# Kernel tuning notes

Hardware: AMD Instinct MI355X
Metric: run time of the kernel (lower is better)

## Reference

```python
import jax, jax.numpy as jnp
import numpy as np

HEADS = 8


def _ln(x, g, b):
    m = x.mean(-1, keepdims=True)
    v = ((x - m) ** 2).mean(-1, keepdims=True)
    return (x - m) / jnp.sqrt(v + 1e-5) * g + b


def _mha(xq, xkv, inw, inb, outw, outb):
    # torch nn.MultiheadAttention (dropout off). xq/xkv: [B,S,D]
    B, S, D = xq.shape
    hd = D // HEADS
    q = (xq @ inw[:D].T + inb[:D]).reshape(B, S, HEADS, hd)
    k = (xkv @ inw[D:2 * D].T + inb[D:2 * D]).reshape(B, S, HEADS, hd)
    v = (xkv @ inw[2 * D:].T + inb[2 * D:]).reshape(B, S, HEADS, hd)
    s = jnp.einsum('bqhd,bkhd->bhqk', q, k) / np.float32(np.sqrt(hd))
    o = jnp.einsum('bhqk,bkhd->bqhd', jax.nn.softmax(s, axis=-1), v).reshape(B, S, D)
    return o @ outw.T + outb


def _eca(x1, x2, qw, qb, kw, kb, vw, vb):
    # EfficientCrossAttention: bmm -> clamp -> softmax -> bmm
    Q = x1 @ qw.T + qb
    K = x2 @ kw.T + kb
    V = x2 @ vw.T + vb
    s = jnp.einsum('bqd,bkd->bqk', Q, K) / np.float32(np.sqrt(Q.shape[-1]))
    s = jnp.clip(s, -100.0, 100.0)
    return jnp.einsum('bqk,bkd->bqd', jax.nn.softmax(s, axis=-1), V)


def _itda(img, caps, qw, qb, kw, kb, vw, vb):
    B, NC, D = caps.shape
    S = img.shape[1]  # 196
    cap_e = jnp.broadcast_to(caps[:, :, None, :], (B, NC, S, D)).reshape(B * NC, S, D)
    img_e = jnp.broadcast_to(img[:, None, :, :], (B, NC, S, D)).reshape(B * NC, S, D)
    out = _eca(cap_e, img_e, qw, qb, kw, kb, vw, vb).reshape(B, NC, S, D)
    mask = (caps.sum(-1) != 0).astype(out.dtype)[:, :, None, None]  # [B,NC,1,1]
    msum = jnp.clip(jnp.broadcast_to(mask, (B, NC, S, 1)).sum(1), 1e-6, None)
    return (out * mask).sum(1) / msum


def _mse(a, b):
    return jnp.mean((a - b) ** 2)


def _forward(input_1, input_2, cap1, cap2, img_w, img_b, w_emb, h_emb,
             mlp_w1, mlp_b1, mlp_w2, mlp_b2, fc_w, fc_b, efc_w, efc_b,
             efc2_w, efc2_b, tr_in_w, tr_in_b, tr_out_w, tr_out_b,
             tr_ln_g, tr_ln_b, itda_qw, itda_qb, itda_kw, itda_kb, itda_vw, itda_vb,
             ca_qw, ca_qb, ca_kw, ca_kb, ca_vw, ca_vb,
             sa_qw, sa_qb, sa_kw, sa_kb, sa_vw, sa_vb):
    B, C, H, W = input_1.shape
    A = img_w.shape[0]
    # caption projections
    cap1_o = cap1 @ fc_w.T + fc_b  # [B,NC,512]
    cap2_o = cap2 @ fc_w.T + fc_b
    cap1_m = jnp.broadcast_to(cap1_o.mean(1)[:, None, :], (B, H * W, A))
    cap2_m = jnp.broadcast_to(cap2_o.mean(1)[:, None, :], (B, H * W, A))
    # 1x1 conv + positional embedding; pe[i,j] = [w_emb[j], h_emb[i]]
    pe = jnp.concatenate([jnp.broadcast_to(w_emb[None, :, :], (W, W, A // 2)),
                          jnp.broadcast_to(h_emb[:, None, :], (H, H, A // 2))], axis=-1)

    def embed(x):
        y = jnp.einsum('bchw,ac->bhwa', x, img_w) + img_b + pe
        return y.reshape(B, H * W, A)

    x1 = embed(input_1)  # [B,196,512]
    x2 = embed(input_2)
    # CDCR (Barlow-Twins style) loss

    def mlp(x):
        return jax.nn.relu(x @ mlp_w1.T + mlp_b1) @ mlp_w2.T + mlp_b2

    f1 = mlp(x1.reshape(-1, A))
    f2 = mlp(x2.reshape(-1, A))
    z_a = (f1 - f1.mean(0)) / jnp.std(f1, axis=0, ddof=1)
    z_b = (f2 - f2.mean(0)) / jnp.std(f2, axis=0, ddof=1)
    Bt, D = z_a.shape
    c = (z_a.T @ z_b) / Bt
    on_diag = jnp.sum((jnp.diagonal(c) - 1.0) ** 2)
    off_diag = jnp.sum(c.reshape(-1)[1:].reshape(D - 1, D + 1)[:, :-1] ** 2)
    cdcr_loss = on_diag + 0.003 * off_diag
    # cross-transformer stack (simultaneous update, as in torch tuple RHS)
    h1, h2 = x1, x2
    for l in range(tr_in_w.shape[0]):
        def layer(q, kv):
            a = _mha(q, kv, tr_in_w[l], tr_in_b[l], tr_out_w[l], tr_out_b[l])
            return _ln(q + a, tr_ln_g[l], tr_ln_b[l])
        h1, h2 = layer(h1, h2), layer(h2, h1)
    diff1 = x1 - h1
    diff2 = x2 - h2
    # ITDA module
    c12 = _eca(diff1, diff2, ca_qw, ca_qb, ca_kw, ca_kb, ca_vw, ca_vb)
    c21 = _eca(diff2, diff1, ca_qw, ca_qb, ca_kw, ca_kb, ca_vw, ca_vb)
    s11 = _eca(diff1, diff1, sa_qw, sa_qb, sa_kw, sa_kb, sa_vw, sa_vb)
    s22 = _eca(diff2, diff2, sa_qw, sa_qb, sa_kw, sa_kb, sa_vw, sa_vb)
    d_bef = _itda(diff1, cap2_o, itda_qw, itda_qb, itda_kw, itda_kb, itda_vw, itda_vb)
    d_aft = _itda(diff2, cap1_o, itda_qw, itda_qb, itda_kw, itda_kb, itda_vw, itda_vb)
    s_bef = _itda(diff1, cap1_o, itda_qw, itda_qb, itda_kw, itda_kb, itda_vw, itda_vb)
    s_aft = _itda(diff2, cap2_o, itda_qw, itda_qb, itda_kw, itda_kb, itda_vw, itda_vb)
    img_to_txt_loss = _mse(d_bef, c12) + _mse(d_aft, c21) + _mse(s_bef, s11) + _mse(s_aft, s22)

    def efc(x):
        return jax.nn.relu(x @ efc_w.T + efc_b)

    dyn = efc(jnp.concatenate([d_bef, d_aft], -1))
    sta = efc(jnp.concatenate([s_bef, s_aft], -1))
    align = efc(jnp.concatenate([dyn, sta], -1))
    txt = efc(jnp.concatenate([cap1_m, cap2_m], -1))
    comb = jnp.concatenate([diff1, diff2, txt, align], -1)  # [B,196,2048]
    out = jax.nn.relu(comb @ efc2_w.T + efc2_b)
    return out, cdcr_loss, img_to_txt_loss


def setup_inputs() -> dict:
    key = jax.random.key(0)
    ks = iter(jax.random.split(key, 64))

    def nrm(shape, s=0.02):
        return jax.random.normal(next(ks), shape, jnp.float32) * s

    B, C, H, W, NC, A = 64, 1024, 14, 14, 16, 512
    inp = dict(
        input_1=jax.random.normal(next(ks), (B, C, H, W), jnp.float32),
        input_2=jax.random.normal(next(ks), (B, C, H, W), jnp.float32),
        cap1=jax.random.normal(next(ks), (B, NC, 768), jnp.float32),
        cap2=jax.random.normal(next(ks), (B, NC, 768), jnp.float32),
        img_w=nrm((A, C)), img_b=jnp.zeros((A,), jnp.float32),
        w_emb=nrm((14, A // 2)), h_emb=nrm((14, A // 2)),
        mlp_w1=nrm((4 * A, A)), mlp_b1=jnp.zeros((4 * A,), jnp.float32),
        mlp_w2=nrm((A, 4 * A)), mlp_b2=jnp.zeros((A,), jnp.float32),
        fc_w=nrm((A, 768)), fc_b=jnp.zeros((A,), jnp.float32),
        efc_w=nrm((A, 2 * A)), efc_b=jnp.zeros((A,), jnp.float32),
        efc2_w=nrm((A, 4 * A)), efc2_b=jnp.zeros((A,), jnp.float32),
        tr_in_w=nrm((2, 3 * A, A)), tr_in_b=jnp.zeros((2, 3 * A), jnp.float32),
        tr_out_w=nrm((2, A, A)), tr_out_b=jnp.zeros((2, A), jnp.float32),
        tr_ln_g=jnp.ones((2, A), jnp.float32), tr_ln_b=jnp.zeros((2, A), jnp.float32),
    )
    for pfx in ('itda', 'ca', 'sa'):
        for nm in ('q', 'k', 'v'):
            inp[pfx + '_' + nm + 'w'] = nrm((A, A))
            inp[pfx + '_' + nm + 'b'] = jnp.zeros((A,), jnp.float32)
    return inp


def reference(input_1, input_2, cap1, cap2, img_w, img_b, w_emb, h_emb,
              mlp_w1, mlp_b1, mlp_w2, mlp_b2, fc_w, fc_b, efc_w, efc_b,
              efc2_w, efc2_b, tr_in_w, tr_in_b, tr_out_w, tr_out_b,
              tr_ln_g, tr_ln_b, itda_qw, itda_qb, itda_kw, itda_kb, itda_vw, itda_vb,
              ca_qw, ca_qb, ca_kw, ca_kb, ca_vw, ca_vb,
              sa_qw, sa_qb, sa_kw, sa_kb, sa_vw, sa_vb):
    return _forward(input_1, input_2, cap1, cap2, img_w, img_b, w_emb, h_emb,
                    mlp_w1, mlp_b1, mlp_w2, mlp_b2, fc_w, fc_b, efc_w, efc_b,
                    efc2_w, efc2_b, tr_in_w, tr_in_b, tr_out_w, tr_out_b,
                    tr_ln_g, tr_ln_b, itda_qw, itda_qb, itda_kw, itda_kb, itda_vw, itda_vb,
                    ca_qw, ca_qb, ca_kw, ca_kb, ca_vw, ca_vb,
                    sa_qw, sa_qb, sa_kw, sa_kb, sa_vw, sa_vb)
```

## Files before the change

kernel.cpp:

```cpp
#include <hip/hip_runtime.h>
#include <hip/hip_bf16.h>
#include <stdint.h>
#include <math.h>

#define BB   64
#define SS   196
#define BS   12544
#define NOUT 6422528L
#define SLD  224

typedef __attribute__((ext_vector_type(8))) short bf16x8;
typedef __attribute__((ext_vector_type(4))) float f32x4;

__device__ __forceinline__ float block_red256(float v, float* red, bool ismax) {
#pragma unroll
  for (int o = 32; o > 0; o >>= 1) {
    float t = __shfl_down(v, o, 64);
    v = ismax ? fmaxf(v, t) : v + t;
  }
  int lane = threadIdx.x & 63, wid = threadIdx.x >> 6;
  if (lane == 0) red[wid] = v;
  __syncthreads();
  float r = ismax ? fmaxf(fmaxf(red[0], red[1]), fmaxf(red[2], red[3]))
                  : (red[0] + red[1]) + (red[2] + red[3]);
// ... 47 lines not shown
  f32x4 acc[4][4] = {};
  float4 xa[4], xw[4], ya[4], yw[4];

  auto ldt = [&](float4 (&ta)[4], float4 (&tw)[4], int t) {
    const float* ap = Ap + t * 32;
    const float* wp = Wp + t * 32;
#pragma unroll
    for (int i = 0; i < 4; ++i) {
      ta[i] = *(const float4*)(ap + i * 4);
      tw[i] = *(const float4*)(wp + i * 4);
    }
  };
  auto stage = [&](float4 (&ta)[4], float4 (&tw)[4], int p) {
    cvt8(&As[p][srow][skh], ta[0], ta[1]);
    cvt8(&As[p][srow][skh + 8], ta[2], ta[3]);
    cvt8(&Bs[p][srow][skh], tw[0], tw[1]);
    cvt8(&Bs[p][srow][skh + 8], tw[2], tw[3]);
  };
  auto step = [&](int t, float4 (&la)[4], float4 (&lw)[4],
                  float4 (&ca)[4], float4 (&cw)[4]) {
    const int par = t & 1;
    if (t + 2 < NK) ldt(la, lw, t + 2);
    bf16x8 af[4], bfr[4];
#pragma unroll
    for (int i = 0; i < 4; ++i) af[i] = *(const bf16x8*)&As[par][wm * 64 + i * 16 + fr][fq * 8];
#pragma unroll
    for (int j = 0; j < 4; ++j) bfr[j] = *(const bf16x8*)&Bs[par][wn * 64 + j * 16 + fr][fq * 8];
    if (t + 1 < NK) stage(ca, cw, par ^ 1);
#pragma unroll
    for (int i = 0; i < 4; ++i)
#pragma unroll
      for (int j = 0; j < 4; ++j)
        acc[i][j] = __builtin_amdgcn_mfma_f32_16x16x32_bf16(af[i], bfr[j], acc[i][j], 0, 0, 0);
    lds_barrier();
  };

  ldt(xa, xw, 0);
  stage(xa, xw, 0);
  if (NK > 1) ldt(xa, xw, 1);
  lds_barrier();
  int t = 0;
  for (; t + 1 < NK; t += 2) { step(t, ya, yw, xa, xw); step(t + 1, xa, xw, ya, yw); }
  if (t < NK) step(t, ya, yw, xa, xw);

  short* Cs = (short*)C;
#pragma unroll
  for (int i = 0; i < 4; ++i) {
    int mB = m0 + wm * 64 + i * 16 + fq * 4;
#pragma unroll
    for (int j = 0; j < 4; ++j) {
      int n = n0 + wn * 64 + j * 16 + fr;
      float bz = bias[n];
#pragma unroll
      for (int r2 = 0; r2 < 4; ++r2) {
        float v = acc[i][j][r2] + bz;
        if (relu) v = fmaxf(v, 0.f);
        if (obf) Cs[(long)(mB + r2) * N + n] = f2bf(v);
        else     C[(long)(mB + r2) * N + n] = v;
      }
    }
  }
}

__global__ __launch_bounds__(256) void k_mfma_embed(
    const float* __restrict__ X1, const float* __restrict__ X2,
    const float* __restrict__ W,
    const float* __restrict__ bias,
    const float* __restrict__ wemb, const float* __restrict__ hemb,
    float* __restrict__ C1, float* __restrict__ C2) {
  __shared__ short As[2][128][40];
  __shared__ short Bs[2][128][40];
  const float* X = blockIdx.z ? X2 : X1;
  float* C = blockIdx.z ? C2 : C1;
  const int tid = threadIdx.x;
  const int lane = tid & 63, wave = tid >> 6;
  const int wm = wave >> 1, wn = wave & 1;
  const int NX = gridDim.x;
  const int wg = xcd_swizzle(blockIdx.y * NX + blockIdx.x, NX * gridDim.y);
  const int m0 = (wg / NX) * 128, n0 = (wg % NX) * 128;
  const int K = 1024, N = 512;
  const int srow = tid >> 1, skh = (tid & 1) * 16;
  const float* Wp = W + (long)(n0 + srow) * K + skh;
  const int arow = tid & 127, khalf = tid >> 7;
  const int am = m0 + arow;
  const int ab = am / 196, as_ = am % 196;
  const float* Xp = X + (long)ab * 200704 + as_;
  const int fr = lane & 15, fq = lane >> 4;
  const int NK = K >> 5;
  f32x4 acc[4][4] = {};
  float xx[16], yx[16];
  float4 xw[4], yw[4];

  auto ldt = [&](float (&tx)[16], float4 (&tw)[4], int t) {
    const int kb = t * 32 + khalf * 16;
#pragma unroll
    for (int i = 0; i < 16; ++i) tx[i] = Xp[(long)(kb + i) * 196];
    const float* wp = Wp + t * 32;
#pragma unroll
    for (int i = 0; i < 4; ++i) tw[i] = *(const float4*)(wp + i * 4);
  };
  auto stage = [&](float (&tx)[16], float4 (&tw)[4], int p) {
    union { short s[16]; int4 v[2]; } u;
#pragma unroll
    for (int i = 0; i < 16; ++i) u.s[i] = f2bf(tx[i]);
    int4* dst = (int4*)&As[p][arow][khalf * 16];
    dst[0] = u.v[0]; dst[1] = u.v[1];
    cvt8(&Bs[p][srow][skh], tw[0], tw[1]);
    cvt8(&Bs[p][srow][skh + 8], tw[2], tw[3]);
  };
  auto step = [&](int t, float (&lx)[16], float4 (&lw)[4],
                  float (&cx)[16], float4 (&cw)[4]) {
    const int par = t & 1;
    if (t + 2 < NK) ldt(lx, lw, t + 2);
    bf16x8 af[4], bfr[4];
#pragma unroll
    for (int i = 0; i < 4; ++i) af[i] = *(const bf16x8*)&As[par][wm * 64 + i * 16 + fr][fq * 8];
#pragma unroll
    for (int j = 0; j < 4; ++j) bfr[j] = *(const bf16x8*)&Bs[par][wn * 64 + j * 16 + fr][fq * 8];
    if (t + 1 < NK) stage(cx, cw, par ^ 1);
#pragma unroll
    for (int i = 0; i < 4; ++i)
#pragma unroll
      for (int j = 0; j < 4; ++j)
        acc[i][j] = __builtin_amdgcn_mfma_f32_16x16x32_bf16(af[i], bfr[j], acc[i][j], 0, 0, 0);
    lds_barrier();
  };

  ldt(xx, xw, 0);
  stage(xx, xw, 0);
  if (NK > 1) ldt(xx, xw, 1);
  lds_barrier();
  int t = 0;
  for (; t + 1 < NK; t += 2) { step(t, yx, yw, xx, xw); step(t + 1, xx, xw, yx, yw); }
  if (t < NK) step(t, yx, yw, xx, xw);

#pragma unroll
  for (int i = 0; i < 4; ++i) {
    int mB = m0 + wm * 64 + i * 16 + fq * 4;
#pragma unroll
    for (int j = 0; j < 4; ++j) {
      int n = n0 + wn * 64 + j * 16 + fr;
      float bz = bias[n];
#pragma unroll
      for (int r2 = 0; r2 < 4; ++r2) {
        int m = mB + r2;
        int s = m % 196;
        float pe = (n < 256) ? wemb[(s % 14) * 256 + n] : hemb[(s / 14) * 256 + (n - 256)];
        C[(long)m * N + n] = acc[i][j][r2] + bz + pe;
      }
    }
  }
}

__global__ __launch_bounds__(256) void k_fmha_bf(
    const short* __restrict__ Q, const short* __restrict__ KV,
    float* __restrict__ O) {
  __shared__ short Vt[64][240];
  __shared__ short Pt[4][16][40];
  const int tid = threadIdx.x;
  const int lane = tid & 63, wave = tid >> 6;
  const int b = blockIdx.x, h = blockIdx.y;
  const long brow = (long)b * 196;
  const short* Qb = Q + brow * 512 + h * 64;
  const short* Kb = KV + brow * 1024 + h * 64;
  const short* Vb = KV + brow * 1024 + 512 + h * 64;
  float* Ob = O + brow * 512 + h * 64;
  const int fr = lane & 15, fq = lane >> 4;

  for (int i = tid; i < 64 * 32; i += 256) {
    int d = i >> 5, k = 192 + (i & 31);
    if (k >= 196) Vt[d][k] = 0;
  }
  for (int i = tid; i < 196 * 8; i += 256) {
    int s = i >> 3, c8 = (i & 7) * 8;
    bf16x8 v = *(const bf16x8*)(Vb + (long)s * 1024 + c8);
#pragma unroll
    for (int j = 0; j < 8; ++j) Vt[c8 + j][s] = v[j];
  }
  __syncthreads();

  for (int qt = wave; qt < 13; qt += 4) {
    const int q0 = qt * 16;
    const int qr = (q0 + fr < 196) ? q0 + fr : 195;
    const short* qp = Qb + (long)qr * 512 + fq * 8;
    bf16x8 aq0 = *(const bf16x8*)(qp);
    bf16x8 aq1 = *(const bf16x8*)(qp + 32);
    f32x4 sc[13];
#pragma unroll
    for (int t = 0; t < 13; ++t) {
      int kr = (t * 16 + fr < 196) ? t * 16 + fr : 195;
      const short* kp = Kb + (long)kr * 1024 + fq * 8;
      bf16x8 bk0 = *(const bf16x8*)(kp);
      bf16x8 bk1 = *(const bf16x8*)(kp + 32);
      f32x4 z = {};
      z = __builtin_amdgcn_mfma_f32_16x16x32_bf16(aq0, bk0, z, 0, 0, 0);
      z = __builtin_amdgcn_mfma_f32_16x16x32_bf16(aq1, bk1, z, 0, 0, 0);
      sc[t] = z;
    }
#pragma unroll
    for (int t = 0; t < 13; ++t)
#pragma unroll
      for (int r2 = 0; r2 < 4; ++r2) sc[t][r2] *= 0.125f;
    if (fr >= 4) {
#pragma unroll
      for (int r2 = 0; r2 < 4; ++r2) sc[12][r2] = -1e30f;
    }
#pragma unroll
    for (int r2 = 0; r2 < 4; ++r2) {
      float m = sc[0][r2];
#pragma unroll
      for (int t = 1; t < 13; ++t) m = fmaxf(m, sc[t][r2]);
#pragma unroll
      for (int o = 1; o < 16; o <<= 1) m = fmaxf(m, __shfl_xor(m, o, 64));
      float s = 0.f;
#pragma unroll
      for (int t = 0; t < 13; ++t) { float e = expf(sc[t][r2] - m); sc[t][r2] = e; s += e; }
#pragma unroll
      for (int o = 1; o < 16; o <<= 1) s += __shfl_xor(s, o, 64);
      float inv = 1.0f / s;
#pragma unroll
      for (int t = 0; t < 13; ++t) sc[t][r2] *= inv;
    }
    f32x4 acc_o[4] = {};
#pragma unroll
    for (int s7 = 0; s7 < 7; ++s7) {
      const int t0 = 2 * s7, t1 = 2 * s7 + 1;
#pragma unroll
      for (int r2 = 0; r2 < 4; ++r2) {
        Pt[wave][fq * 4 + r2][fr] = f2bf(sc[t0][r2]);
        Pt[wave][fq * 4 + r2][16 + fr] = (t1 < 13) ? f2bf(sc[t1][r2]) : (short)0;
      }
      asm volatile("s_waitcnt lgkmcnt(0)" ::: "memory");
      bf16x8 ap = *(const bf16x8*)&Pt[wave][fr][fq * 8];
#pragma unroll
      for (int dt = 0; dt < 4; ++dt) {
        bf16x8 bv = *(const bf16x8*)&Vt[dt * 16 + fr][32 * s7 + fq * 8];
        acc_o[dt] = __builtin_amdgcn_mfma_f32_16x16x32_bf16(ap, bv, acc_o[dt], 0, 0, 0);
      }
    }
#pragma unroll
    for (int r2 = 0; r2 < 4; ++r2) {
      int qrow = q0 + fq * 4 + r2;
      if (qrow < 196) {
        float* op = Ob + (long)qrow * 512;
#pragma unroll
        for (int dt = 0; dt < 4; ++dt) op[dt * 16 + fr] = acc_o[dt][r2];
      }
    }
  }
}

__global__ __launch_bounds__(256) void k_mfma_bnt(
    const float* __restrict__ A, const float* __restrict__ B, float* __restrict__ C,
    int M, int N, int K, int lda, int ldb, int ldc, int nz2,
    int64_t sA1, int64_t sA2, int64_t sB1, int64_t sB2, int64_t sC1, int64_t sC2,
    float scale, int clampf, const float* __restrict__ bias2, int relu2) {
  __shared__ short As[2][64][40];
  __shared__ short Bs[2][64][40];
  const int tid = threadIdx.x;
  const int lane = tid & 63, wave = tid >> 6;
  const int NX = gridDim.x;
  const int wg = xcd_swizzle(blockIdx.y * NX + blockIdx.x, NX * gridDim.y);
  const int m0 = (wg / NX) * 64, n0 = (wg % NX) * 64;
  const int z = blockIdx.z, z1 = z / nz2, z2 = z % nz2;
  const float* Ab = A + z1 * sA1 + z2 * sA2;
  const float* Bb = B + z1 * sB1 + z2 * sB2;
  float* Cb = C + z1 * sC1 + z2 * sC2;
  const int sr = tid >> 2, skh = (tid & 3) * 8;
  const int ar = (m0 + sr < M) ? m0 + sr : M - 1;
  const int br = (n0 + sr < N) ? n0 + sr : N - 1;
  const float* Ap = Ab + (long)ar * lda + skh;
  const float* Bp = Bb + (long)br * ldb + skh;
  const int fr = lane & 15, fq = lane >> 4;
  const int NK = K >> 5;
  f32x4 acc[4] = {};
  float4 xa[2], xb[2], ya[2], yb[2];

  auto ldt = [&](float4 (&ta)[2], float4 (&tb)[2], int t) {
    const int kb = t * 32;
#pragma unroll
    for (int i = 0; i < 2; ++i) {
      ta[i] = *(const float4*)(Ap + kb + i * 4);
      tb[i] = *(const float4*)(Bp + kb + i * 4);
    }
  };
  auto stage = [&](float4 (&ta)[2], float4 (&tb)[2], int p) {
    cvt8(&As[p][sr][skh], ta[0], ta[1]);
    cvt8(&Bs[p][sr][skh], tb[0], tb[1]);
  };
  auto step = [&](int t, float4 (&la)[2], float4 (&lb)[2],
                  float4 (&ca)[2], float4 (&cb)[2]) {
    const int par = t & 1;
    if (t + 2 < NK) ldt(la, lb, t + 2);
    bf16x8 bfr = *(const bf16x8*)&Bs[par][wave * 16 + fr][fq * 8];
    bf16x8 af[4];
#pragma unroll
    for (int i = 0; i < 4; ++i) af[i] = *(const bf16x8*)&As[par][i * 16 + fr][fq * 8];
    if (t + 1 < NK) stage(ca, cb, par ^ 1);
#pragma unroll
    for (int i = 0; i < 4; ++i)
      acc[i] = __builtin_amdgcn_mfma_f32_16x16x32_bf16(af[i], bfr, acc[i], 0, 0, 0);
    lds_barrier();
  };

  ldt(xa, xb, 0);
  stage(xa, xb, 0);
  if (NK > 1) ldt(xa, xb, 1);
  lds_barrier();
  int t = 0;
  for (; t + 1 < NK; t += 2) { step(t, ya, yb, xa, xb); step(t + 1, xa, xb, ya, yb); }
  if (t < NK) step(t, ya, yb, xa, xb);

  const int n = n0 + wave * 16 + fr;
  if (n < N) {
    float bz = bias2 ? bias2[n] : 0.f;
#pragma unroll
    for (int i = 0; i < 4; ++i) {
      int mb = m0 + i * 16 + fq * 4;
#pragma unroll
      for (int r2 = 0; r2 < 4; ++r2) {
        int m = mb + r2;
        if (m < M) {
          float v = acc[i][r2] * scale + bz;
          if (relu2) v = fmaxf(v, 0.f);
          if (clampf) v = fminf(fmaxf(v, -100.f), 100.f);
          Cb[(long)m * ldc + n] = v;
        }
      }
    }
  }
}

__global__ __launch_bounds__(256) void k_mfma_bnt_abf(
    const short* __restrict__ A, const float* __restrict__ B, float* __restrict__ C,
    int M, int N, int K, int lda, int ldb, int ldc,
    const float* __restrict__ bias2, int relu2) {
  __shared__ short As[2][64][40];
  __shared__ short Bs[2][64][40];
  const int tid = threadIdx.x;
  const int lane = tid & 63, wave = tid >> 6;
  const int NX = gridDim.x;
  const int wg = xcd_swizzle(blockIdx.y * NX + blockIdx.x, NX * gridDim.y);
  const int m0 = (wg / NX) * 64, n0 = (wg % NX) * 64;
  const int sr = tid >> 2, skh = (tid & 3) * 8;
  const int ar = (m0 + sr < M) ? m0 + sr : M - 1;
  const int br = (n0 + sr < N) ? n0 + sr : N - 1;
  const short* Ap = A + (long)ar * lda + skh;
  const float* Bp = B + (long)br * ldb + skh;
  const int fr = lane & 15, fq = lane >> 4;
  const int NK = K >> 5;
  f32x4 acc[4] = {};
  int4 xa, ya;
  float4 xb[2], yb[2];

  auto ldt = [&](int4& ta, float4 (&tb)[2], int t) {
    const int kb = t * 32;
    ta = *(const int4*)(Ap + kb);
#pragma unroll
    for (int i = 0; i < 2; ++i) tb[i] = *(const float4*)(Bp + kb + i * 4);
  };
  auto stage = [&](int4& ta, float4 (&tb)[2], int p) {
    *(int4*)&As[p][sr][skh] = ta;
    cvt8(&Bs[p][sr][skh], tb[0], tb[1]);
  };
  auto step = [&](int t, int4& la, float4 (&lb)[2], int4& ca, float4 (&cb)[2]) {
    const int par = t & 1;
    if (t + 2 < NK) ldt(la, lb, t + 2);
    bf16x8 bfr = *(const bf16x8*)&Bs[par][wave * 16 + fr][fq * 8];
    bf16x8 af[4];
#pragma unroll
    for (int i = 0; i < 4; ++i) af[i] = *(const bf16x8*)&As[par][i * 16 + fr][fq * 8];
    if (t + 1 < NK) stage(ca, cb, par ^ 1);
#pragma unroll
    for (int i = 0; i < 4; ++i)
      acc[i] = __builtin_amdgcn_mfma_f32_16x16x32_bf16(af[i], bfr, acc[i], 0, 0, 0);
    lds_barrier();
  };

  ldt(xa, xb, 0);
  stage(xa, xb, 0);
  if (NK > 1) ldt(xa, xb, 1);
  lds_barrier();
  int t = 0;
  for (; t + 1 < NK; t += 2) { step(t, ya, yb, xa, xb); step(t + 1, xa, xb, ya, yb); }
  if (t < NK) step(t, ya, yb, xa, xb);

  const int n = n0 + wave * 16 + fr;
  if (n < N) {
    float bz = bias2 ? bias2[n] : 0.f;
#pragma unroll
    for (int i = 0; i < 4; ++i) {
      int mb = m0 + i * 16 + fq * 4;
#pragma unroll
      for (int r2 = 0; r2 < 4; ++r2) {
        int m = mb + r2;
        if (m < M) {
          float v = acc[i][r2] + bz;
          if (relu2) v = fmaxf(v, 0.f);
          C[(long)m * ldc + n] = v;
// ... 188 lines not shown
}

__global__ void k_zero(float* __restrict__ p, int n) {
  int i = blockIdx.x * 256 + threadIdx.x;
  if (i < n) p[i] = 0.f;
}

__global__ __launch_bounds__(256) void k_diff(
    float* __restrict__ d, const float* __restrict__ x, const float* __restrict__ h) {
  long i = ((long)blockIdx.x * 256 + threadIdx.x) * 4;
  float4 xv = *(const float4*)(x + i);
  float4 hv = *(const float4*)(h + i);
  float4 r; r.x = xv.x - hv.x; r.y = xv.y - hv.y; r.z = xv.z - hv.z; r.w = xv.w - hv.w;
  *(float4*)(d + i) = r;
}

__global__ __launch_bounds__(256) void k_catkv(
    float* __restrict__ dw, const float* __restrict__ kw, const float* __restrict__ vw,
    float* __restrict__ db, const float* __restrict__ kb, const float* __restrict__ vb) {
  int i = blockIdx.x * 256 + threadIdx.x;
  int r = i >> 9;
  dw[i] = (r < 512) ? kw[i] : vw[i - 262144];
  if (i < 1024) db[i] = (i < 512) ? kb[i] : vb[i - 512];
}

__global__ __launch_bounds__(256) void k_colstats(
    const float* __restrict__ f, float* __restrict__ sums, float* __restrict__ sqs) {
  int c = blockIdx.x * 32 + (threadIdx.x & 31);
  int rbase = blockIdx.y * 256;
  int r0 = rbase + (threadIdx.x >> 5);
  float s = 0.f, s2 = 0.f;
  for (int r = r0; r < rbase + 256; r += 8) {
    float v = f[(long)r * 512 + c];
    s += v; s2 += v * v;
  }
  __shared__ float sh[256], sh2[256];
  sh[threadIdx.x] = s; sh2[threadIdx.x] = s2;
  __syncthreads();
  if (threadIdx.x < 32) {
    for (int i = 1; i < 8; ++i) { s += sh[i * 32 + threadIdx.x]; s2 += sh2[i * 32 + threadIdx.x]; }
    atomicAdd(&sums[c], s);
    atomicAdd(&sqs[c], s2);
  }
}

__global__ void k_finstats(const float* __restrict__ sums, const float* __restrict__ sqs,
                           float* __restrict__ mean, float* __restrict__ istd) {
  int c = blockIdx.x * 256 + threadIdx.x;
  float mu = sums[c] / 12544.0f;
  float var = (sqs[c] - 12544.0f * mu * mu) / 12543.0f;
  mean[c] = mu;
  istd[c] = 1.0f / sqrtf(var);
}

__global__ __launch_bounds__(256) void k_znorm(float* __restrict__ f, const float* __restrict__ mean,
                                               const float* __restrict__ istd) {
  long i = (long)blockIdx.x * 256 + threadIdx.x;
  int c = (int)(i & 511);
  f[i] = (f[i] - mean[c]) * istd[c];
}

__global__ __launch_bounds__(256) void k_cdcr_part(const float* __restrict__ Cm,
                                                   double* __restrict__ part) {
  int base = blockIdx.x * 1024;
  double on = 0, off = 0;
  for (int i = base + threadIdx.x; i < base + 1024; i += 256) {
    float v = Cm[i];
    int r = i >> 9, c = i & 511;
    if (r == c) { double d = (double)v - 1.0; on += d * d; }
    else        { off += (double)v * (double)v; }
  }
  __shared__ double s_on[256], s_off[256];
  s_on[threadIdx.x] = on; s_off[threadIdx.x] = off;
  __syncthreads();
  for (int st = 128; st > 0; st >>= 1) {
    if (threadIdx.x < st) { s_on[threadIdx.x] += s_on[threadIdx.x + st]; s_off[threadIdx.x] += s_off[threadIdx.x + st]; }
    __syncthreads();
  }
  if (threadIdx.x == 0) { part[blockIdx.x] = s_on[0]; part[256 + blockIdx.x] = s_off[0]; }
}

__global__ void k_cdcr_fin(const double* __restrict__ part, float* __restrict__ out) {
  __shared__ double s_on[256], s_off[256];
  s_on[threadIdx.x] = part[threadIdx.x];
  s_off[threadIdx.x] = part[256 + threadIdx.x];
  __syncthreads();
  for (int st = 128; st > 0; st >>= 1) {
    if (threadIdx.x < st) { s_on[threadIdx.x] += s_on[threadIdx.x + st]; s_off[threadIdx.x] += s_off[threadIdx.x + st]; }
    __syncthreads();
  }
  if (threadIdx.x == 0) out[0] = (float)(s_on[0] + 0.003 * s_off[0]);
}

__global__ __launch_bounds__(64) void k_mask(const float* __restrict__ capo, float* __restrict__ mask) {
  int pidx = blockIdx.x;
  float s = 0.f;
  for (int i = threadIdx.x; i < 512; i += 64) s += capo[(long)pidx * 512 + i];
#pragma unroll
  for (int o = 32; o > 0; o >>= 1) s += __shfl_down(s, o, 64);
  if (threadIdx.x == 0) mask[pidx] = (s != 0.f) ? 1.f : 0.f;
}

__global__ __launch_bounds__(256) void k_meannc(const float* __restrict__ src, const float* __restrict__ mask,
                                                float* __restrict__ vec) {
  int d = blockIdx.x * 256 + threadIdx.x;
  int b = blockIdx.y;
  float acc = 0.f, ms = 0.f;
  for (int nc = 0; nc < 16; ++nc) {
    float mk = mask ? mask[b * 16 + nc] : 1.f;
    acc += src[((long)b * 16 + nc) * 512 + d] * mk;
    ms += mk;
  }
  vec[(long)b * 512 + d] = acc / fmaxf(ms, 1e-6f);
}

__global__ __launch_bounds__(256) void k_mse(const float* __restrict__ full, const float* __restrict__ vec,
                                             double* __restrict__ part) {
  double loc = 0;
  const long n = NOUT;
  for (long i = (long)blockIdx.x * 256 + threadIdx.x; i < n; i += 256L * 1024) {
    int d = (int)(i & 511);
    int b = (int)(i >> 9) / 196;
    float df = full[i] - vec[b * 512 + d];
    loc += (double)df * (double)df;
  }
  __shared__ double sh[256];
  sh[threadIdx.x] = loc;
  __syncthreads();
  for (int st = 128; st > 0; st >>= 1) {
    if (threadIdx.x < st) sh[threadIdx.x] += sh[threadIdx.x + st];
    __syncthreads();
  }
  if (threadIdx.x == 0) part[blockIdx.x] = sh[0];
}

__global__ void k_finloss(const double* __restrict__ part, float* __restrict__ out) {
  __shared__ double sh[256];
  double s = 0;
  for (int i = threadIdx.x; i < 4096; i += 256) s += part[i];
  sh[threadIdx.x] = s;
  __syncthreads();
  for (int st = 128; st > 0; st >>= 1) {
    if (threadIdx.x < st) sh[threadIdx.x] += sh[threadIdx.x + st];
    __syncthreads();
  }
  if (threadIdx.x == 0) out[0] = (float)(sh[0] / (64.0 * 196.0 * 512.0));
}

__global__ __launch_bounds__(256) void k_concat2(float* __restrict__ dst, const float* __restrict__ a,
                                                 const float* __restrict__ b) {
  int i = blockIdx.x * 256 + threadIdx.x;
  int col = i & 1023, row = i >> 10;
  dst[i] = (col < 512) ? a[row * 512 + col] : b[row * 512 + col - 512];
}

__global__ __launch_bounds__(256) void k_comb_bf(
    short* __restrict__ dst, const float* __restrict__ d1, const float* __restrict__ d2,
    const float* __restrict__ txt, const float* __restrict__ al) {
  long i = (long)blockIdx.x * 256 + threadIdx.x;
  int col = (int)(i & 2047);
  long m = i >> 11;
  int b = (int)(m / 196);
  float v;
  if (col < 512)       v = d1[m * 512 + col];
  else if (col < 1024) v = d2[m * 512 + col - 512];
  else if (col < 1536) v = txt[(long)b * 512 + col - 1024];
  else                 v = al[(long)b * 512 + col - 1536];
  dst[i] = f2bf(v);
}

extern "C" void kernel_launch(void* const* d_in, const int* in_sizes, int n_in,
                              void* d_out, int out_size, void* d_ws, size_t ws_size,
                              hipStream_t stream) {
  (void)in_sizes; (void)n_in; (void)out_size; (void)ws_size;
  const float* in1    = (const float*)d_in[0];
  const float* in2    = (const float*)d_in[1];
  const float* cap1   = (const float*)d_in[2];
  const float* cap2   = (const float*)d_in[3];
  const float* imgw   = (const float*)d_in[4];
  const float* imgb   = (const float*)d_in[5];
  const float* wemb   = (const float*)d_in[6];
  const float* hemb   = (const float*)d_in[7];
  const float* mlpw1  = (const float*)d_in[8];
  const float* mlpb1  = (const float*)d_in[9];
  const float* mlpw2  = (const float*)d_in[10];
  const float* mlpb2  = (const float*)d_in[11];
  const float* fcw    = (const float*)d_in[12];
  const float* fcb    = (const float*)d_in[13];
  const float* efcw   = (const float*)d_in[14];
  const float* efcb   = (const float*)d_in[15];
  const float* efc2w  = (const float*)d_in[16];
  const float* efc2b  = (const float*)d_in[17];
  const float* trinw  = (const float*)d_in[18];
  const float* trinb  = (const float*)d_in[19];
  const float* troutw = (const float*)d_in[20];
  const float* troutb = (const float*)d_in[21];
  const float* trlng  = (const float*)d_in[22];
  const float* trlnb  = (const float*)d_in[23];
  const float* itqw = (const float*)d_in[24]; const float* itqb = (const float*)d_in[25];
  const float* itkw = (const float*)d_in[26]; const float* itkb = (const float*)d_in[27];
  const float* itvw = (const float*)d_in[28]; const float* itvb = (const float*)d_in[29];
  const float* caqw = (const float*)d_in[30]; const float* caqb = (const float*)d_in[31];
  const float* cakw = (const float*)d_in[32]; const float* cakb = (const float*)d_in[33];
  const float* cavw = (const float*)d_in[34]; const float* cavb = (const float*)d_in[35];
  const float* saqw = (const float*)d_in[36]; const float* saqb = (const float*)d_in[37];
  const float* sakw = (const float*)d_in[38]; const float* sakb = (const float*)d_in[39];
  const float* savw = (const float*)d_in[40]; const float* savb = (const float*)d_in[41];

  float* out = (float*)d_out;

  const size_t SZ = (size_t)BS * 512;
  float* w = (float*)d_ws;
  auto alloc = [&](size_t n) { float* p = w; w += n; return p; };
  float* h1 = alloc(SZ);
  float* h2 = alloc(SZ);
  float* tA = alloc(SZ);
  float* tB = alloc(SZ);
  float* tC = alloc(SZ);
  float* tD = alloc(SZ);
  float* sbuf = alloc(SZ);
  float* cap1o = alloc(64 * 16 * 512);
  float* cap2o = alloc(64 * 16 * 512);
  float* qc1   = alloc(64 * 16 * 512);
  float* qc2   = alloc(64 * 16 * 512);
  float* attb  = alloc(64 * 16 * 512);
  float* attb2 = alloc(64 * 16 * 512);
  float* cmat  = alloc(512 * 512);
  float* colsum1 = alloc(512); float* colsq1 = alloc(512);
  float* colsum2 = alloc(512); float* colsq2 = alloc(512);
  float* mean1 = alloc(512); float* istd1 = alloc(512);
  float* mean2 = alloc(512); float* istd2 = alloc(512);
  float* mask1 = alloc(1024); float* mask2 = alloc(1024);
  float* vdbef = alloc(64 * 512); float* vdaft = alloc(64 * 512);
  float* vsbef = alloc(64 * 512); float* vsaft = alloc(64 * 512);
  float* cm1 = alloc(64 * 512); float* cm2 = alloc(64 * 512);
  float* vdyn = alloc(64 * 512); float* vsta = alloc(64 * 512);
  float* valign = alloc(64 * 512); float* vtxt = alloc(64 * 512);
  float* ccat = alloc(64 * 1024);
  double* msepart = (double*)alloc(4096 * 2);
  double* cdcrpart = (double*)alloc(1024);
  float* itkvw = alloc(1024 * 512); float* itkvb = alloc(1024);
  float* cakvw = alloc(1024 * 512); float* cakvb = alloc(1024);
  float* sakvw = alloc(1024 * 512); float* sakvb = alloc(1024);
  float* x1 = alloc(2 * SZ);
  float* x2 = x1 + SZ;

  auto gemm = [&](const float* Aa, const float* Ww, const float* bb, float* Cc,
                  int M, int N, int K, int relu) {
    long g128 = ((M % 128) == 0 && (N % 128) == 0) ? (long)(N / 128) * (M / 128) : 0;
    if (g128 >= 784 && (K % 32) == 0)
      k_mfma_nt<<<dim3(N / 128, M / 128), 256, 0, stream>>>(Aa, Ww, bb, Cc, M, N, K, relu, 0);
    else
      k_mfma_bnt<<<dim3(N / 64, (M + 63) / 64, 1), 256, 0, stream>>>(
          Aa, Ww, Cc, M, N, K, K, K, N, 1,
          0, 0, 0, 0, 0, 0, 1.0f, 0, bb, relu);
  };
  const int64_t RB = (int64_t)SS * 512;
  const int64_t QB = 16 * 512;
  auto attn512 = [&](const float* Qp, int64_t qZ1, int64_t qZ2, const float* KVp, int64_t kvZ,
                     float* Op, int64_t oZ1, int64_t oZ2, int M, int zq, float scale) {
    int mt = (M + 63) / 64;
    int64_t sS2 = (int64_t)M * SLD;
    int64_t sS1 = 64 * sS2;
    k_mfma_bnt<<<dim3(4, mt, 64 * zq), 256, 0, stream>>>(
        Qp, KVp, sbuf, M, 196, 512, 512, 1024, SLD, 64,
        qZ1, qZ2, 0, kvZ, sS1, sS2, scale, 1, nullptr, 0);
    k_softmax_rows<<<(64 * zq * M + 3) / 4, 256, 0, stream>>>(sbuf, 64 * zq * M);
    k_mfma_bnn<<<dim3(8, mt, 64 * zq), 256, 0, stream>>>(
        sbuf, KVp + 512, Op, M, 512, SLD, 196, SLD, 1024, 512, 64,
        sS1, sS2, 0, kvZ, oZ1, oZ2);
  };
  auto attn_mha = [&](const short* Qp, const short* KVp, float* Op) {
    k_fmha_bf<<<dim3(64, 8), 256, 0, stream>>>(Qp, KVp, Op);
  };
  auto efc64 = [&](const float* Aa, float* Cc) {
    k_mfma_bnt<<<dim3(8, 1, 1), 256, 0, stream>>>(
        Aa, efcw, Cc, 64, 512, 1024, 1024, 1024, 512, 1,
        0, 0, 0, 0, 0, 0, 1.0f, 0, efcb, 1);
  };

  const float scalE = 1.0f / sqrtf(512.0f);

  k_catkv<<<2048, 256, 0, stream>>>(itkvw, itkw, itvw, itkvb, itkb, itvb);
  k_catkv<<<2048, 256, 0, stream>>>(cakvw, cakw, cavw, cakvb, cakb, cavb);
  k_catkv<<<2048, 256, 0, stream>>>(sakvw, sakw, savw, sakvb, sakb, savb);

  k_mfma_embed<<<dim3(4, BS / 128, 2), 256, 0, stream>>>(
      in1, in2, imgw, imgb, wemb, hemb, x1, x2);
  gemm(cap1, fcw, fcb, cap1o, 1024, 512, 768, 0);
  gemm(cap2, fcw, fcb, cap2o, 1024, 512, 768, 0);
  k_meannc<<<dim3(2, 64), 256, 0, stream>>>(cap1o, nullptr, cm1);
  k_meannc<<<dim3(2, 64), 256, 0, stream>>>(cap2o, nullptr, cm2);

  k_mfma_nt<<<dim3(16, 98), 256, 0, stream>>>(x1, mlpw1, mlpb1, tC, BS, 2048, 512, 1, 1);
  k_mfma_bnt_abf<<<dim3(8, 196), 256, 0, stream>>>(
      (const short*)tC, mlpw2, tA, BS, 512, 2048, 2048, 2048, 512, mlpb2, 0);
  k_mfma_nt<<<dim3(16, 98), 256, 0, stream>>>(x2, mlpw1, mlpb1, tC, BS, 2048, 512, 1, 1);
  k_mfma_bnt_abf<<<dim3(8, 196), 256, 0, stream>>>(
      (const short*)tC, mlpw2, tB, BS, 512, 2048, 2048, 2048, 512, mlpb2, 0);
  k_zero<<<8, 256, 0, stream>>>(colsum1, 2048);
  k_colstats<<<dim3(16, 49), 256, 0, stream>>>(tA, colsum1, colsq1);
  k_colstats<<<dim3(16, 49), 256, 0, stream>>>(tB, colsum2, colsq2);
  k_finstats<<<2, 256, 0, stream>>>(colsum1, colsq1, mean1, istd1);
  k_finstats<<<2, 256, 0, stream>>>(colsum2, colsq2, mean2, istd2);
  k_znorm<<<25088, 256, 0, stream>>>(tA, mean1, istd1);
  k_znorm<<<25088, 256, 0, stream>>>(tB, mean2, istd2);
  k_zero<<<1024, 256, 0, stream>>>(cmat, 262144);
  k_mfma_corr<<<dim3(8, 8, 14), 256, 0, stream>>>(tA, tB, cmat, BS / 14, 1.0f / (float)BS);
  k_cdcr_part<<<256, 256, 0, stream>>>(cmat, cdcrpart);
  k_cdcr_fin<<<1, 256, 0, stream>>>(cdcrpart, out + NOUT);

  for (int l = 0; l < 2; ++l) {
    const float* Wq = trinw + (size_t)l * 1536 * 512;
    const float* Wkv = Wq + 512 * 512;
    const float* bq = trinb + l * 1536;
    const float* bkv = bq + 512;
    const float* Wo = troutw + (size_t)l * 512 * 512;
    const float* bo = troutb + l * 512;
    const float* g  = trlng + l * 512;
    const float* be = trlnb + l * 512;
    const float* s1 = l ? h1 : x1;
    const float* s2 = l ? h2 : x2;
    k_mfma_nt<<<dim3(4, 196), 256, 0, stream>>>(s1, Wq, bq, tA, 2 * BS, 512, 512, 0, 1);
    k_mfma_nt<<<dim3(8, 98), 256, 0, stream>>>(s2, Wkv, bkv, tC, BS, 1024, 512, 0, 1);
    k_mfma_nt<<<dim3(8, 98), 256, 0, stream>>>(s1, Wkv, bkv, tD, BS, 1024, 512, 0, 1);
    attn_mha((const short*)tA, (const short*)tC, tB);
    k_mfma_bnt<<<dim3(8, 196, 1), 256, 0, stream>>>(tB, Wo, sbuf, BS, 512, 512, 512, 512, 512, 1,
                                                    0, 0, 0, 0, 0, 0, 1.0f, 0, bo, 0);
    k_addln2<<<BS, 256, 0, stream>>>(h1, s1, sbuf, g, be);
    attn_mha((const short*)tA + (size_t)BS * 512, (const short*)tD, tB);
    k_mfma_bnt<<<dim3(8, 196, 1), 256, 0, stream>>>(tB, Wo, sbuf, BS, 512, 512, 512, 512, 512, 1,
                                                    0, 0, 0, 0, 0, 0, 1.0f, 0, bo, 0);
    k_addln2<<<BS, 256, 0, stream>>>(h2, s2, sbuf, g, be);
  }

  k_diff<<<12544, 256, 0, stream>>>(tC, x1, h1);

  gemm(cap1o, itqw, itqb, qc1, 2048, 512, 512, 0);
  k_mask<<<1024, 64, 0, stream>>>(cap1o, mask1);
  k_mask<<<1024, 64, 0, stream>>>(cap2o, mask2);
  gemm(tC, itkvw, itkvb, tA, BS, 1024, 512, 0);
  attn512(qc1, 524288, QB, tA, 2 * RB, attb, 524288, QB, 16, 2, scalE);
  k_meannc<<<dim3(2, 64), 256, 0, stream>>>(attb,  mask1, vsbef);
  k_meannc<<<dim3(2, 64), 256, 0, stream>>>(attb2, mask2, vdbef);
  gemm(tD, itkvw, itkvb, tA, BS, 1024, 512, 0);
  attn512(qc1, 524288, QB, tA, 2 * RB, attb, 524288, QB, 16, 2, scalE);
  k_meannc<<<dim3(2, 64), 256, 0, stream>>>(attb,  mask1, vdaft);
  k_meannc<<<dim3(2, 64), 256, 0, stream>>>(attb2, mask2, vsaft);

  auto eca_mse = [&](const float* xq, const float* xkv,
                     const float* qw2, const float* qb2,
                     const float* kvw2, const float* kvb2,
                     const float* vec, double* part) {
    gemm(xq,  qw2, qb2, h1, BS, 512, 512, 0);
    gemm(xkv, kvw2, kvb2, tA, BS, 1024, 512, 0);
    attn512(h1, 0, RB, tA, 2 * RB, h2, 0, RB, 196, 1, scalE);
    k_mse<<<1024, 256, 0, stream>>>(h2, vec, part);
  };
  eca_mse(tC, tD, caqw, caqb, cakvw, cakvb, vdbef, msepart);
  eca_mse(tD, tC, caqw, caqb, cakvw, cakvb, vdaft, msepart + 1024);
  eca_mse(tC, tC, saqw, saqb, sakvw, sakvb, vsbef, msepart + 2048);
  eca_mse(tD, tD, saqw, saqb, sakvw, sakvb, vsaft, msepart + 3072);
  k_finloss<<<1, 256, 0, stream>>>(msepart, out + NOUT + 1);

  k_concat2<<<256, 256, 0, stream>>>(ccat, vdbef, vdaft);
  efc64(ccat, vdyn);
  k_concat2<<<256, 256, 0, stream>>>(ccat, vsbef, vsaft);
  efc64(ccat, vsta);
  k_concat2<<<256, 256, 0, stream>>>(ccat, vdyn, vsta);
  efc64(ccat, valign);
  k_concat2<<<256, 256, 0, stream>>>(ccat, cm1, cm2);
  efc64(ccat, vtxt);

  k_comb_bf<<<100352, 256, 0, stream>>>((short*)h1, tC, tD, vtxt, valign);
  k_mfma_bnt_abf<<<dim3(8, 196), 256, 0, stream>>>(
      (const short*)h1, efc2w, out, BS, 512, 2048, 2048, 2048, 512, efc2b, 1);
}
```

Measured before the change: 2.383 ms.

## Batch paired branches into double-size GEMMs and attention launches

Merges the two image branches into single launches: the MLP, the KV projection, MHA (a z-dimension selects the KV source), the output projection, the add+LN, the ITDA KV GEMM, and the ECA pairs. The three independent efc GEMMs are stacked into one M=192 launch. MHA now writes bf16 output, which the bf16-A GEMM consumes, halving that intermediate's traffic. This cuts launch count and raises per-launch parallelism, at the cost of heavy buffer aliasing (negative strides, reused workspace regions) that is easy to get wrong.

```diff
diff --git a/kernel.cpp b/kernel.cpp
--- a/kernel.cpp
+++ b/kernel.cpp
@@ -223,19 +223,21 @@
   }
 }
 
-__global__ __launch_bounds__(256) void k_fmha_bf(
-    const short* __restrict__ Q, const short* __restrict__ KV,
-    float* __restrict__ O) {
+__global__ __launch_bounds__(256) void k_fmha_bf2(
+    const short* __restrict__ Q, const short* __restrict__ KVd1,
+    const short* __restrict__ KVd2, short* __restrict__ O) {
   __shared__ short Vt[64][240];
   __shared__ short Pt[4][16][40];
   const int tid = threadIdx.x;
   const int lane = tid & 63, wave = tid >> 6;
-  const int b = blockIdx.x, h = blockIdx.y;
+  const int b = blockIdx.x, h = blockIdx.y, z = blockIdx.z;
+  const short* KV = z ? KVd2 : KVd1;
   const long brow = (long)b * 196;
-  const short* Qb = Q + brow * 512 + h * 64;
+  const size_t zo = (size_t)z * BS * 512;
+  const short* Qb = Q + zo + brow * 512 + h * 64;
   const short* Kb = KV + brow * 1024 + h * 64;
   const short* Vb = KV + brow * 1024 + 512 + h * 64;
-  float* Ob = O + brow * 512 + h * 64;
+  short* Ob = O + zo + brow * 512 + h * 64;
   const int fr = lane & 15, fq = lane >> 4;
 
   for (int i = tid; i < 64 * 32; i += 256) {
@@ -263,10 +265,10 @@
       const short* kp = Kb + (long)kr * 1024 + fq * 8;
       bf16x8 bk0 = *(const bf16x8*)(kp);
       bf16x8 bk1 = *(const bf16x8*)(kp + 32);
-      f32x4 z = {};
-      z = __builtin_amdgcn_mfma_f32_16x16x32_bf16(aq0, bk0, z, 0, 0, 0);
-      z = __builtin_amdgcn_mfma_f32_16x16x32_bf16(aq1, bk1, z, 0, 0, 0);
-      sc[t] = z;
+      f32x4 zz = {};
+      zz = __builtin_amdgcn_mfma_f32_16x16x32_bf16(aq0, bk0, zz, 0, 0, 0);
+      zz = __builtin_amdgcn_mfma_f32_16x16x32_bf16(aq1, bk1, zz, 0, 0, 0);
+      sc[t] = zz;
     }
 #pragma unroll
     for (int t = 0; t < 13; ++t)
@@ -313,9 +315,9 @@
     for (int r2 = 0; r2 < 4; ++r2) {
       int qrow = q0 + fq * 4 + r2;
       if (qrow < 196) {
-        float* op = Ob + (long)qrow * 512;
-#pragma unroll
-        for (int dt = 0; dt < 4; ++dt) op[dt * 16 + fr] = acc_o[dt][r2];
+        short* op = Ob + (long)qrow * 512;
+#pragma unroll
+        for (int dt = 0; dt < 4; ++dt) op[dt * 16 + fr] = f2bf(acc_o[dt][r2]);
       }
     }
   }
@@ -810,6 +812,19 @@
   int i = blockIdx.x * 256 + threadIdx.x;
   int col = i & 1023, row = i >> 10;
   dst[i] = (col < 512) ? a[row * 512 + col] : b[row * 512 + col - 512];
+}
+
+__global__ __launch_bounds__(256) void k_concat6(
+    float* __restrict__ dst,
+    const float* __restrict__ a0, const float* __restrict__ b0,
+    const float* __restrict__ a1, const float* __restrict__ b1,
+    const float* __restrict__ a2, const float* __restrict__ b2) {
+  int i = blockIdx.x * 256 + threadIdx.x;
+  int col = i & 1023, row = i >> 10;
+  int grp = row >> 6, r = row & 63;
+  const float* a = grp == 0 ? a0 : (grp == 1 ? a1 : a2);
+  const float* b = grp == 0 ? b0 : (grp == 1 ? b1 : b2);
+  dst[i] = (col < 512) ? a[r * 512 + col] : b[r * 512 + col - 512];
 }
 
 __global__ __launch_bounds__(256) void k_comb_bf(
@@ -868,6 +883,7 @@
   float* out = (float*)d_out;
 
   const size_t SZ = (size_t)BS * 512;
+  const int64_t SZl = (int64_t)SZ;
   float* w = (float*)d_ws;
   auto alloc = [&](size_t n) { float* p = w; w += n; return p; };
   float* h1 = alloc(SZ);
@@ -893,8 +909,8 @@
   float* vsbef = alloc(64 * 512); float* vsaft = alloc(64 * 512);
   float* cm1 = alloc(64 * 512); float* cm2 = alloc(64 * 512);
   float* vdyn = alloc(64 * 512); float* vsta = alloc(64 * 512);
-  float* valign = alloc(64 * 512); float* vtxt = alloc(64 * 512);
-  float* ccat = alloc(64 * 1024);
+  float* vtxt = alloc(64 * 512); float* valign = alloc(64 * 512);
+  float* ccat = alloc(192 * 1024);
   double* msepart = (double*)alloc(4096 * 2);
   double* cdcrpart = (double*)alloc(1024);
   float* itkvw = alloc(1024 * 512); float* itkvb = alloc(1024);
@@ -915,25 +931,23 @@
   };
   const int64_t RB = (int64_t)SS * 512;
   const int64_t QB = 16 * 512;
-  auto attn512 = [&](const float* Qp, int64_t qZ1, int64_t qZ2, const float* KVp, int64_t kvZ,
+  auto attn512 = [&](const float* Qp, int64_t qZ1, int64_t qZ2,
+                     const float* KVp, int64_t kvZ1, int64_t kvZ2,
                      float* Op, int64_t oZ1, int64_t oZ2, int M, int zq, float scale) {
     int mt = (M + 63) / 64;
     int64_t sS2 = (int64_t)M * SLD;
     int64_t sS1 = 64 * sS2;
     k_mfma_bnt<<<dim3(4, mt, 64 * zq), 256, 0, stream>>>(
         Qp, KVp, sbuf, M, 196, 512, 512, 1024, SLD, 64,
-        qZ1, qZ2, 0, kvZ, sS1, sS2, scale, 1, nullptr, 0);
+        qZ1, qZ2, kvZ1, kvZ2, sS1, sS2, scale, 1, nullptr, 0);
     k_softmax_rows<<<(64 * zq * M + 3) / 4, 256, 0, stream>>>(sbuf, 64 * zq * M);
     k_mfma_bnn<<<dim3(8, mt, 64 * zq), 256, 0, stream>>>(
         sbuf, KVp + 512, Op, M, 512, SLD, 196, SLD, 1024, 512, 64,
-        sS1, sS2, 0, kvZ, oZ1, oZ2);
-  };
-  auto attn_mha = [&](const short* Qp, const short* KVp, float* Op) {
-    k_fmha_bf<<<dim3(64, 8), 256, 0, stream>>>(Qp, KVp, Op);
-  };
-  auto efc64 = [&](const float* Aa, float* Cc) {
-    k_mfma_bnt<<<dim3(8, 1, 1), 256, 0, stream>>>(
-        Aa, efcw, Cc, 64, 512, 1024, 1024, 1024, 512, 1,
+        sS1, sS2, kvZ1, kvZ2, oZ1, oZ2);
+  };
+  auto efcM = [&](const float* Aa, float* Cc, int M) {
+    k_mfma_bnt<<<dim3(8, (M + 63) / 64, 1), 256, 0, stream>>>(
+        Aa, efcw, Cc, M, 512, 1024, 1024, 1024, 512, 1,
         0, 0, 0, 0, 0, 0, 1.0f, 0, efcb, 1);
   };
 
@@ -950,21 +964,18 @@
   k_meannc<<<dim3(2, 64), 256, 0, stream>>>(cap1o, nullptr, cm1);
   k_meannc<<<dim3(2, 64), 256, 0, stream>>>(cap2o, nullptr, cm2);
 
-  k_mfma_nt<<<dim3(16, 98), 256, 0, stream>>>(x1, mlpw1, mlpb1, tC, BS, 2048, 512, 1, 1);
-  k_mfma_bnt_abf<<<dim3(8, 196), 256, 0, stream>>>(
-      (const short*)tC, mlpw2, tA, BS, 512, 2048, 2048, 2048, 512, mlpb2, 0);
-  k_mfma_nt<<<dim3(16, 98), 256, 0, stream>>>(x2, mlpw1, mlpb1, tC, BS, 2048, 512, 1, 1);
-  k_mfma_bnt_abf<<<dim3(8, 196), 256, 0, stream>>>(
-      (const short*)tC, mlpw2, tB, BS, 512, 2048, 2048, 2048, 512, mlpb2, 0);
+  k_mfma_nt<<<dim3(16, 196), 256, 0, stream>>>(x1, mlpw1, mlpb1, tA, 2 * BS, 2048, 512, 1, 1);
+  k_mfma_bnt_abf<<<dim3(8, 392), 256, 0, stream>>>(
+      (const short*)tA, mlpw2, h1, 2 * BS, 512, 2048, 2048, 2048, 512, mlpb2, 0);
   k_zero<<<8, 256, 0, stream>>>(colsum1, 2048);
-  k_colstats<<<dim3(16, 49), 256, 0, stream>>>(tA, colsum1, colsq1);
-  k_colstats<<<dim3(16, 49), 256, 0, stream>>>(tB, colsum2, colsq2);
+  k_colstats<<<dim3(16, 49), 256, 0, stream>>>(h1, colsum1, colsq1);
+  k_colstats<<<dim3(16, 49), 256, 0, stream>>>(h2, colsum2, colsq2);
   k_finstats<<<2, 256, 0, stream>>>(colsum1, colsq1, mean1, istd1);
   k_finstats<<<2, 256, 0, stream>>>(colsum2, colsq2, mean2, istd2);
-  k_znorm<<<25088, 256, 0, stream>>>(tA, mean1, istd1);
-  k_znorm<<<25088, 256, 0, stream>>>(tB, mean2, istd2);
+  k_znorm<<<25088, 256, 0, stream>>>(h1, mean1, istd1);
+  k_znorm<<<25088, 256, 0, stream>>>(h2, mean2, istd2);
   k_zero<<<1024, 256, 0, stream>>>(cmat, 262144);
-  k_mfma_corr<<<dim3(8, 8, 14), 256, 0, stream>>>(tA, tB, cmat, BS / 14, 1.0f / (float)BS);
+  k_mfma_corr<<<dim3(8, 8, 14), 256, 0, stream>>>(h1, h2, cmat, BS / 14, 1.0f / (float)BS);
   k_cdcr_part<<<256, 256, 0, stream>>>(cmat, cdcrpart);
   k_cdcr_fin<<<1, 256, 0, stream>>>(cdcrpart, out + NOUT);
 
@@ -978,18 +989,14 @@
     const float* g  = trlng + l * 512;
     const float* be = trlnb + l * 512;
     const float* s1 = l ? h1 : x1;
-    const float* s2 = l ? h2 : x2;
     k_mfma_nt<<<dim3(4, 196), 256, 0, stream>>>(s1, Wq, bq, tA, 2 * BS, 512, 512, 0, 1);
-    k_mfma_nt<<<dim3(8, 98), 256, 0, stream>>>(s2, Wkv, bkv, tC, BS, 1024, 512, 0, 1);
-    k_mfma_nt<<<dim3(8, 98), 256, 0, stream>>>(s1, Wkv, bkv, tD, BS, 1024, 512, 0, 1);
-    attn_mha((const short*)tA, (const short*)tC, tB);
-    k_mfma_bnt<<<dim3(8, 196, 1), 256, 0, stream>>>(tB, Wo, sbuf, BS, 512, 512, 512, 512, 512, 1,
-                                                    0, 0, 0, 0, 0, 0, 1.0f, 0, bo, 0);
-    k_addln2<<<BS, 256, 0, stream>>>(h1, s1, sbuf, g, be);
-    attn_mha((const short*)tA + (size_t)BS * 512, (const short*)tD, tB);
-    k_mfma_bnt<<<dim3(8, 196, 1), 256, 0, stream>>>(tB, Wo, sbuf, BS, 512, 512, 512, 512, 512, 1,
-                                                    0, 0, 0, 0, 0, 0, 1.0f, 0, bo, 0);
-    k_addln2<<<BS, 256, 0, stream>>>(h2, s2, sbuf, g, be);
+    k_mfma_nt<<<dim3(8, 196), 256, 0, stream>>>(s1, Wkv, bkv, tC, 2 * BS, 1024, 512, 0, 1);
+    k_fmha_bf2<<<dim3(64, 8, 2), 256, 0, stream>>>(
+        (const short*)tA, (const short*)tC + (size_t)BS * 1024, (const short*)tC,
+        (short*)sbuf);
+    k_mfma_bnt_abf<<<dim3(8, 392), 256, 0, stream>>>(
+        (const short*)sbuf, Wo, tB, 2 * BS, 512, 512, 512, 512, 512, bo, 0);
+    k_addln2<<<2 * BS, 256, 0, stream>>>(h1, s1, tB, g, be);
   }
 
   k_diff<<<12544, 256, 0, stream>>>(tC, x1, h1);
@@ -997,38 +1004,35 @@
   gemm(cap1o, itqw, itqb, qc1, 2048, 512, 512, 0);
   k_mask<<<1024, 64, 0, stream>>>(cap1o, mask1);
   k_mask<<<1024, 64, 0, stream>>>(cap2o, mask2);
-  gemm(tC, itkvw, itkvb, tA, BS, 1024, 512, 0);
-  attn512(qc1, 524288, QB, tA, 2 * RB, attb, 524288, QB, 16, 2, scalE);
+  gemm(tC, itkvw, itkvb, h1, 2 * BS, 1024, 512, 0);
+  attn512(qc1, 524288, QB, h1, 0, 2 * RB, attb, 524288, QB, 16, 2, scalE);
   k_meannc<<<dim3(2, 64), 256, 0, stream>>>(attb,  mask1, vsbef);
   k_meannc<<<dim3(2, 64), 256, 0, stream>>>(attb2, mask2, vdbef);
-  gemm(tD, itkvw, itkvb, tA, BS, 1024, 512, 0);
-  attn512(qc1, 524288, QB, tA, 2 * RB, attb, 524288, QB, 16, 2, scalE);
+  attn512(qc1, 524288, QB, h1 + 2 * SZ, 0, 2 * RB, attb, 524288, QB, 16, 2, scalE);
   k_meannc<<<dim3(2, 64), 256, 0, stream>>>(attb,  mask1, vdaft);
   k_meannc<<<dim3(2, 64), 256, 0, stream>>>(attb2, mask2, vsaft);
 
-  auto eca_mse = [&](const float* xq, const float* xkv,
-                     const float* qw2, const float* qb2,
-                     const float* kvw2, const float* kvb2,
-                     const float* vec, double* part) {
-    gemm(xq,  qw2, qb2, h1, BS, 512, 512, 0);
-    gemm(xkv, kvw2, kvb2, tA, BS, 1024, 512, 0);
-    attn512(h1, 0, RB, tA, 2 * RB, h2, 0, RB, 196, 1, scalE);
-    k_mse<<<1024, 256, 0, stream>>>(h2, vec, part);
-  };
-  eca_mse(tC, tD, caqw, caqb, cakvw, cakvb, vdbef, msepart);
-  eca_mse(tD, tC, caqw, caqb, cakvw, cakvb, vdaft, msepart + 1024);
-  eca_mse(tC, tC, saqw, saqb, sakvw, sakvb, vsbef, msepart + 2048);
-  eca_mse(tD, tD, saqw, saqb, sakvw, sakvb, vsaft, msepart + 3072);
+  auto eca_pair = [&](const float* qw2, const float* qb2,
+                      const float* kvw2, const float* kvb2,
+                      const float* kvbase, int64_t kvZ1,
+                      const float* vec0, double* part0,
+                      const float* vec1, double* part1) {
+    gemm(tC, qw2, qb2, x1, 2 * BS, 512, 512, 0);
+    gemm(tC, kvw2, kvb2, h1, 2 * BS, 1024, 512, 0);
+    attn512(x1, SZl, RB, kvbase, kvZ1, 2 * RB, x1, SZl, RB, 196, 2, scalE);
+    k_mse<<<1024, 256, 0, stream>>>(x1, vec0, part0);
+    k_mse<<<1024, 256, 0, stream>>>(x1 + SZ, vec1, part1);
+  };
+  eca_pair(caqw, caqb, cakvw, cakvb, h1 + 2 * SZ, -2 * SZl,
+           vdbef, msepart, vdaft, msepart + 1024);
+  eca_pair(saqw, saqb, sakvw, sakvb, h1, 2 * SZl,
+           vsbef, msepart + 2048, vsaft, msepart + 3072);
   k_finloss<<<1, 256, 0, stream>>>(msepart, out + NOUT + 1);
 
-  k_concat2<<<256, 256, 0, stream>>>(ccat, vdbef, vdaft);
-  efc64(ccat, vdyn);
-  k_concat2<<<256, 256, 0, stream>>>(ccat, vsbef, vsaft);
-  efc64(ccat, vsta);
+  k_concat6<<<768, 256, 0, stream>>>(ccat, vdbef, vdaft, vsbef, vsaft, cm1, cm2);
+  efcM(ccat, vdyn, 192);
   k_concat2<<<256, 256, 0, stream>>>(ccat, vdyn, vsta);
-  efc64(ccat, valign);
-  k_concat2<<<256, 256, 0, stream>>>(ccat, cm1, cm2);
-  efc64(ccat, vtxt);
+  efcM(ccat, valign, 64);
 
   k_comb_bf<<<100352, 256, 0, stream>>>((short*)h1, tC, tD, vtxt, valign);
   k_mfma_bnt_abf<<<dim3(8, 196), 256, 0, stream>>>(
```

Result: faster. 2.177 ms (-8.6%).
